# Optimization experiments

Measured on AMD Instinct MI355X. Metric: run time of the kernel, lower is better.

The kernel has to match this reference:

```python
import jax, jax.numpy as jnp
import numpy as np

B, S, W, D, T = 64, 512, 384, 768, 21


def setup_inputs() -> dict:
    key = jax.random.key(0)
    ks = jax.random.split(key, 8)
    hidden_states = jax.random.normal(ks[0], (B, S, D), dtype=jnp.float32)  # BERT last_hidden_state
    word_maps = jnp.sort(jax.random.randint(ks[1], (B, W), 0, S), axis=1)  # first-subword index per word
    tags = jax.random.randint(ks[2], (B, W), 0, T)
    word_mask = jnp.ones((B, W), dtype=bool)  # torchcrf requires mask[:,0] all on
    W_tag = jax.random.normal(ks[3], (T, D), dtype=jnp.float32) * 0.02  # hidden2tag weight
    b_tag = jnp.zeros((T,), dtype=jnp.float32)
    start_trans = jax.random.uniform(ks[4], (T,), minval=-0.1, maxval=0.1)
    end_trans = jax.random.uniform(ks[5], (T,), minval=-0.1, maxval=0.1)
    trans = jax.random.uniform(ks[6], (T, T), minval=-0.1, maxval=0.1)
    return dict(hidden_states=hidden_states, W_tag=W_tag, b_tag=b_tag,
                start_trans=start_trans, end_trans=end_trans, trans=trans,
                word_maps=word_maps, tags=tags, word_mask=word_mask)


def reference(hidden_states, W_tag, b_tag, start_trans, end_trans, trans,
              word_maps, tags, word_mask):
    # --- ragged subword -> word gather (vectorized form of the python loop) ---
    word_feats = jnp.take_along_axis(hidden_states, word_maps[:, :, None], axis=1)  # [B,W,D]
    # dropout is identity in eval / deterministic reference
    emissions = jnp.einsum('bwd,td->bwt', word_feats, W_tag) + b_tag  # [B,W,T]

    maskf = word_mask.astype(emissions.dtype)
    bidx = jnp.arange(tags.shape[0])

    # --- CRF numerator: score of the given tag sequence ---
    emit_sc = jnp.take_along_axis(emissions, tags[:, :, None], axis=2)[..., 0]  # [B,W]
    trans_sc = trans[tags[:, :-1], tags[:, 1:]]                                  # [B,W-1]
    num = start_trans[tags[:, 0]] + emit_sc[:, 0]
    num = num + jnp.sum((trans_sc + emit_sc[:, 1:]) * maskf[:, 1:], axis=1)
    lengths = word_mask.sum(axis=1)
    last_tags = jnp.take_along_axis(tags, (lengths - 1)[:, None], axis=1)[:, 0]
    num = num + end_trans[last_tags]

    # --- CRF denominator: log partition via forward recurrence (scan over time) ---
    def step(score, xm):
        em_t, m_t = xm  # [B,T], [B]
        nxt = jax.nn.logsumexp(score[:, :, None] + trans[None, :, :] + em_t[:, None, :], axis=1)
        return jnp.where(m_t[:, None], nxt, score), None

    score0 = start_trans[None, :] + emissions[:, 0]  # [B,T]
    score, _ = jax.lax.scan(step, score0,
                            (jnp.swapaxes(emissions[:, 1:], 0, 1), word_mask[:, 1:].T))
    log_z = jax.nn.logsumexp(score + end_trans[None, :], axis=1)  # [B]

    llh = num - log_z
    return -jnp.mean(llh)  # reduction='mean', negated
```

## Files before the change

### kernel.cpp

```cpp
#include <hip/hip_runtime.h>
#include <math.h>

#define BB 64
#define SS 512
#define WW 384
#define DD 768
#define TT 21
#define ROWS (BB*WW)
#define EMSTRIDE (WW*TT)
#define NCH 32
#define CLEN 12
#define PSTRIDE 24
#define LSTR 28
#define PTSZ (PSTRIDE*PSTRIDE)
#define LN32 3.4657359027997265f

typedef short   bf16x8 __attribute__((ext_vector_type(8)));
typedef float   f32x4  __attribute__((ext_vector_type(4)));
union FragU { bf16x8 v; unsigned u[4]; };

__device__ __forceinline__ unsigned pack_bf16(unsigned lo, unsigned hi) {
    return __builtin_amdgcn_perm(hi, lo, 0x07060302);
}

__global__ __launch_bounds__(256) void emissions_kernel(
    const float* __restrict__ hidden, const int* __restrict__ word_maps,
    const float* __restrict__ W_tag, const float* __restrict__ b_tag,
    float* __restrict__ em, float* __restrict__ out)
{
    __shared__ __align__(16) unsigned short Bs[24 * 2 * 4 * 16 * 8];
    __shared__ __align__(16) float Sred[2][64][8];
    __shared__ int rowoff[32];

    const int tid = threadIdx.x;
    const int rowBase = blockIdx.x * 32;

    if (blockIdx.x == 0 && tid == 0) out[0] = 0.0f;

    if (tid < 32) {
        int row = rowBase + tid;
        int b = row / WW;
        int w = row - b * WW;
        rowoff[tid] = b * SS + word_maps[b * WW + w];
    }

    for (int i = tid; i < TT * (DD / 4); i += 256) {
        int t = i / (DD / 4), q = i - t * (DD / 4);
        int k  = q * 4;
        int ks = k >> 5, quad = (k >> 3) & 3, e = k & 7;
        int nt = t >> 4, l16 = t & 15;
        float4 wv = *(const float4*)&W_tag[t * DD + k];
        int off = ((ks * 2 + nt) * 4 + quad) * 128 + l16 * 8 + e;
        *(unsigned*)&Bs[off]     = pack_bf16(__float_as_uint(wv.x), __float_as_uint(wv.y));
        *(unsigned*)&Bs[off + 2] = pack_bf16(__float_as_uint(wv.z), __float_as_uint(wv.w));
    }
    __syncthreads();

    const int wv_  = tid >> 6;
    const int rt   = wv_ >> 1;
    const int h    = wv_ & 1;
    const int lane = tid & 63;
    const int l16  = lane & 15;
    const int quad = lane >> 4;

    const float* abase = hidden + (size_t)rowoff[rt * 16 + l16] * DD
                                + h * (DD / 2) + quad * 8;
    const unsigned short* bbase = Bs + quad * 128 + l16 * 8 + h * 12 * 1024;

    f32x4 acc0 = {}, acc1 = {};

    float4 A0[4], A1[4];
    #pragma unroll
    for (int p = 0; p < 4; ++p) {
        A0[p] = *(const float4*)(abase + p * 32);
        A1[p] = *(const float4*)(abase + p * 32 + 4);
    }
    bf16x8 b0c = *(const bf16x8*)(bbase);
    bf16x8 b1c = *(const bf16x8*)(bbase + 512);

    #pragma unroll
    for (int ks = 0; ks < 12; ++ks) {
        bf16x8 b0n = b0c, b1n = b1c;
        if (ks < 11) {
            b0n = *(const bf16x8*)(bbase + (ks + 1) * 1024);
            b1n = *(const bf16x8*)(bbase + (ks + 1) * 1024 + 512);
        }
        FragU a;
        a.u[0] = pack_bf16(__float_as_uint(A0[ks & 3].x), __float_as_uint(A0[ks & 3].y));
        a.u[1] = pack_bf16(__float_as_uint(A0[ks & 3].z), __float_as_uint(A0[ks & 3].w));
        a.u[2] = pack_bf16(__float_as_uint(A1[ks & 3].x), __float_as_uint(A1[ks & 3].y));
        a.u[3] = pack_bf16(__float_as_uint(A1[ks & 3].z), __float_as_uint(A1[ks & 3].w));
        if (ks < 8) {
            A0[ks & 3] = *(const float4*)(abase + (ks + 4) * 32);
            A1[ks & 3] = *(const float4*)(abase + (ks + 4) * 32 + 4);
        }
        acc0 = __builtin_amdgcn_mfma_f32_16x16x32_bf16(a.v, b0c, acc0, 0, 0, 0);
        acc1 = __builtin_amdgcn_mfma_f32_16x16x32_bf16(a.v, b1c, acc1, 0, 0, 0);
        b0c = b0n; b1c = b1n;
    }

    if (h == 1) {
        #pragma unroll
        for (int r = 0; r < 4; ++r) {
            Sred[rt][lane][r]     = acc0[r];
            Sred[rt][lane][r + 4] = acc1[r];
        }
    }
    __syncthreads();

    if (h == 0) {
        #pragma unroll
        for (int r = 0; r < 4; ++r) {
            acc0[r] += Sred[rt][lane][r];
            acc1[r] += Sred[rt][lane][r + 4];
        }
        int rbase = rowBase + rt * 16 + quad * 4;
        {
            float bt = b_tag[l16];
            #pragma unroll
            for (int r = 0; r < 4; ++r)
                em[(size_t)(rbase + r) * TT + l16] = acc0[r] + bt;
        }
        if (16 + l16 < TT) {
            float bt = b_tag[16 + l16];
            #pragma unroll
            for (int r = 0; r < 4; ++r)
                em[(size_t)(rbase + r) * TT + 16 + l16] = acc1[r] + bt;
        }
    }
}

__global__ __launch_bounds__(256, 2) void chunk_kernel(
    const float* __restrict__ em, const float* __restrict__ trans,
    float* __restrict__ Pmat)
{
    __shared__ __align__(16) float Es[24 * LSTR];
    __shared__ __align__(16) float Pbuf[4][2][21 * LSTR];
    __shared__ __align__(16) float gem[4][CLEN * LSTR];

    const int tid  = threadIdx.x;
    const int wid  = tid >> 6;
    const int lane = tid & 63;
    const int id   = blockIdx.x * 4 + wid;
    const int b    = id / NCH;
    const int c    = id - b * NCH;
    const int s0   = 1 + c * CLEN;
    const int n    = (c == NCH - 1) ? (WW - s0) : CLEN;

    for (int idx = tid; idx < 24 * LSTR; idx += 256) {
        int k = idx / LSTR, j = idx - k * LSTR;
        Es[idx] = (k < TT && j < TT) ? __expf(trans[k * TT + j]) * 0.03125f : 0.f;
    }

    int i3r = lane / 6;
    const int jg  = lane - i3r * 6;
    const bool active = (i3r < 7) && (jg < 6);
    const int i3 = (i3r < 7) ? i3r : 6;
    const int jbase = (jg < 6 ? jg : 5) * 4;

    for (int idx = lane; idx < n * LSTR; idx += 64) {
        int tt = idx / LSTR, j = idx - tt * LSTR;
        float g = 1.0f;
        if (j < TT) g = __expf(em[((size_t)b * WW + (s0 + tt)) * TT + j]);
        gem[wid][idx] = g;
    }
    __syncthreads();

    float4 Er[24];
    #pragma unroll
    for (int k = 0; k < 24; ++k)
        Er[k] = *(const float4*)&Es[k * LSTR + jbase];

    {
        float4 g = *(const float4*)&gem[wid][jbase];
        #pragma unroll
        for (int r = 0; r < 3; ++r) {
            int i = i3 * 3 + r;
            float4 e = *(const float4*)&Es[i * LSTR + jbase];
            float4 v = make_float4(e.x * g.x, e.y * g.y, e.z * g.z, e.w * g.w);
            if (active) *(float4*)&Pbuf[wid][0][i * LSTR + jbase] = v;
        }
    }

    int pp = 0;
    for (int tt = 1; tt < n; ++tt) {
        float acc[3][4];
        #pragma unroll
        for (int r = 0; r < 3; ++r)
            #pragma unroll
            for (int q = 0; q < 4; ++q) acc[r][q] = 0.f;

        const float* Pc = &Pbuf[wid][pp][0];
        #pragma unroll
        for (int kb = 0; kb < 6; ++kb) {
            float4 p0 = *(const float4*)&Pc[(i3 * 3 + 0) * LSTR + kb * 4];
            float4 p1 = *(const float4*)&Pc[(i3 * 3 + 1) * LSTR + kb * 4];
            float4 p2 = *(const float4*)&Pc[(i3 * 3 + 2) * LSTR + kb * 4];
            #pragma unroll
            for (int kk = 0; kk < 4; ++kk) {
                float4 e = Er[kb * 4 + kk];
                float a = (kk == 0) ? p0.x : (kk == 1) ? p0.y : (kk == 2) ? p0.z : p0.w;
                float bv= (kk == 0) ? p1.x : (kk == 1) ? p1.y : (kk == 2) ? p1.z : p1.w;
                float cv= (kk == 0) ? p2.x : (kk == 1) ? p2.y : (kk == 2) ? p2.z : p2.w;
                acc[0][0] = fmaf(a, e.x, acc[0][0]); acc[0][1] = fmaf(a, e.y, acc[0][1]);
                acc[0][2] = fmaf(a, e.z, acc[0][2]); acc[0][3] = fmaf(a, e.w, acc[0][3]);
                acc[1][0] = fmaf(bv, e.x, acc[1][0]); acc[1][1] = fmaf(bv, e.y, acc[1][1]);
                acc[1][2] = fmaf(bv, e.z, acc[1][2]); acc[1][3] = fmaf(bv, e.w, acc[1][3]);
                acc[2][0] = fmaf(cv, e.x, acc[2][0]); acc[2][1] = fmaf(cv, e.y, acc[2][1]);
                acc[2][2] = fmaf(cv, e.z, acc[2][2]); acc[2][3] = fmaf(cv, e.w, acc[2][3]);
            }
        }
        float4 g = *(const float4*)&gem[wid][tt * LSTR + jbase];
        if (active) {
            #pragma unroll
            for (int r = 0; r < 3; ++r) {
                float4 v = make_float4(acc[r][0] * g.x, acc[r][1] * g.y,
                                       acc[r][2] * g.z, acc[r][3] * g.w);
                *(float4*)&Pbuf[wid][1 - pp][(i3 * 3 + r) * LSTR + jbase] = v;
            }
        }
        pp ^= 1;
    }

    float* dst = Pmat + (size_t)id * PTSZ;
    const float* Pf = &Pbuf[wid][pp][0];
    for (int idx = lane; idx < PTSZ; idx += 64) {
        int j = idx / PSTRIDE, i = idx - j * PSTRIDE;
        dst[idx] = (i < TT) ? Pf[i * LSTR + j] : 0.f;
    }
}

__device__ __forceinline__ float lane_bcast(float v, int l) {
    return __uint_as_float(__builtin_amdgcn_readlane(__float_as_uint(v), l));
}

#define LOADC(q0,q1,q2,q3,q4,q5,cc) { \
    const float* Pp = Pb + (size_t)(cc) * PTSZ; \
    q0 = *(const float4*)&Pp[0];  q1 = *(const float4*)&Pp[4]; \
    q2 = *(const float4*)&Pp[8];  q3 = *(const float4*)&Pp[12]; \
    q4 = *(const float4*)&Pp[16]; q5 = Pp[20]; }

#define MERGE(c_, q0,q1,q2,q3,q4,q5) { \
    float col[TT]; \
    col[0]=q0.x;  col[1]=q0.y;  col[2]=q0.z;  col[3]=q0.w; \
    col[4]=q1.x;  col[5]=q1.y;  col[6]=q1.z;  col[7]=q1.w; \
    col[8]=q2.x;  col[9]=q2.y;  col[10]=q2.z; col[11]=q2.w; \
    col[12]=q3.x; col[13]=q3.y; col[14]=q3.z; col[15]=q3.w; \
    col[16]=q4.x; col[17]=q4.y; col[18]=q4.z; col[19]=q4.w; \
    col[20]=q5; \
    float p0 = 0.f, p1 = 0.f, p2 = 0.f; \
    _Pragma("unroll") \
    for (int i = 0; i < TT; i += 3) { \
        p0 = fmaf(lane_bcast(sig, i    ), col[i    ], p0); \
        p1 = fmaf(lane_bcast(sig, i + 1), col[i + 1], p1); \
        p2 = fmaf(lane_bcast(sig, i + 2), col[i + 2], p2); \
    } \
    float v = act ? (p0 + p1 + p2) : 0.0f; \
    float m = v; \
    _Pragma("unroll") \
    for (int o = 32; o > 0; o >>= 1) m = fmaxf(m, __shfl_xor(m, o)); \
    int nst = ((c_) == NCH - 1) ? (WW - (1 + (c_) * CLEN)) : CLEN; \
    M += __logf(m) + (float)nst * LN32; \
    sig = v / m; }

__global__ __launch_bounds__(64, 1) void combine_kernel(
    const float* __restrict__ Pmat, const float* __restrict__ em,
    const int* __restrict__ tags, const float* __restrict__ start_trans,
    const float* __restrict__ end_trans, const float* __restrict__ trans,
    float* __restrict__ out)
{
    const int b = blockIdx.x;
    const int j = threadIdx.x;
    const bool act = (j < TT);
    const int jc = act ? j : (TT - 1);
    const float* emb = em + (size_t)b * EMSTRIDE;
    const float* Pb = Pmat + (size_t)b * NCH * PTSZ + jc * PSTRIDE;

    float4 A0,A1,A2,A3,A4; float A5;
    float4 B0,B1,B2,B3,B4; float B5;
    float4 C0,C1,C2,C3,C4; float C5;
    float4 D0,D1,D2,D3,D4; float D5;
    LOADC(A0,A1,A2,A3,A4,A5, 0);
    LOADC(B0,B1,B2,B3,B4,B5, 1);
    LOADC(C0,C1,C2,C3,C4,C5, 2);
    LOADC(D0,D1,D2,D3,D4,D5, 3);

    float s0v = start_trans[jc] + emb[jc];
    float M = act ? s0v : -1e30f;
    #pragma unroll
    for (int o = 32; o > 0; o >>= 1) M = fmaxf(M, __shfl_xor(M, o));
    float sig = act ? __expf(s0v - M) : 0.0f;

    for (int c = 0; c < NCH; c += 4) {
        MERGE(c,     A0,A1,A2,A3,A4,A5);
        if (c + 4 < NCH) LOADC(A0,A1,A2,A3,A4,A5, c + 4);
        MERGE(c + 1, B0,B1,B2,B3,B4,B5);
        if (c + 5 < NCH) LOADC(B0,B1,B2,B3,B4,B5, c + 5);
        MERGE(c + 2, C0,C1,C2,C3,C4,C5);
        if (c + 6 < NCH) LOADC(C0,C1,C2,C3,C4,C5, c + 6);
        MERGE(c + 3, D0,D1,D2,D3,D4,D5);
        if (c + 7 < NCH) LOADC(D0,D1,D2,D3,D4,D5, c + 7);
    }

    float fin = (act && sig > 0.f) ? (M + __logf(sig) + end_trans[jc]) : -1e30f;
    float mm = fin;
    #pragma unroll
    for (int o = 32; o > 0; o >>= 1) mm = fmaxf(mm, __shfl_xor(mm, o));
    float pe = __expf(fin - mm);
    float ssum = pe;
    #pragma unroll
    for (int o = 32; o > 0; o >>= 1) ssum += __shfl_xor(ssum, o);
    float lz = mm + __logf(ssum);

    const int* tb = tags + b * WW;
    float part = 0.f;
    #pragma unroll
    for (int w = j; w < WW; w += 64) {
        int tw = tb[w];
        float e = emb[w * TT + tw];
        float tsc = (w == 0) ? start_trans[tw] : trans[tb[w - 1] * TT + tw];
        part += tsc + e;
    }
    #pragma unroll
    for (int o = 32; o > 0; o >>= 1) part += __shfl_xor(part, o);

    if (j == 0) {
        float num = part + end_trans[tb[WW - 1]];
        atomicAdd(out, -(num - lz) * (1.0f / BB));
    }
}

extern "C" void kernel_launch(void* const* d_in, const int* in_sizes, int n_in,
                              void* d_out, int out_size, void* d_ws, size_t ws_size,
                              hipStream_t stream) {
    const float* hidden      = (const float*)d_in[0];
    const float* W_tag       = (const float*)d_in[1];
    const float* b_tag       = (const float*)d_in[2];
    const float* start_trans = (const float*)d_in[3];
    const float* end_trans   = (const float*)d_in[4];
    const float* trans       = (const float*)d_in[5];
    const int*   word_maps   = (const int*)  d_in[6];
    const int*   tags        = (const int*)  d_in[7];

    float* out  = (float*)d_out;
    float* em   = (float*)d_ws;
    float* Pmat = (float*)d_ws + (size_t)ROWS * TT;

    emissions_kernel<<<ROWS / 32, 256, 0, stream>>>(hidden, word_maps, W_tag, b_tag, em, out);
    chunk_kernel<<<BB * NCH / 4, 256, 0, stream>>>(em, trans, Pmat);
    combine_kernel<<<BB, 64, 0, stream>>>(Pmat, em, tags, start_trans, end_trans, trans, out);
}
```

Measured before the change: 196.9 us.

## Fuse combine kernel into chunk kernel via last-block-done counter per batch

Drops the separate combine kernel launch. Each chunk block bumps a per-batch atomic counter after writing its partial transfer matrices, and the last of the 8 blocks for that batch runs the merge and log-likelihood reduction. The emissions kernel zeroes the counters. This removes one kernel launch and its dependency gap. The cost is a threadfence, an extra barrier, and a serial merge tail running on a single wave.

Result: slower. 238.2 us (+21.0%).

```diff
diff --git a/kernel.cpp b/kernel.cpp
--- a/kernel.cpp
+++ b/kernel.cpp
@@ -26,7 +26,7 @@
 __global__ __launch_bounds__(256) void emissions_kernel(
     const float* __restrict__ hidden, const int* __restrict__ word_maps,
     const float* __restrict__ W_tag, const float* __restrict__ b_tag,
-    float* __restrict__ em, float* __restrict__ out)
+    float* __restrict__ em, float* __restrict__ out, int* __restrict__ cnt)
 {
     __shared__ __align__(16) unsigned short Bs[24 * 2 * 4 * 16 * 8];
     __shared__ __align__(16) float Sred[2][64][8];
@@ -35,7 +35,10 @@
     const int tid = threadIdx.x;
     const int rowBase = blockIdx.x * 32;
 
-    if (blockIdx.x == 0 && tid == 0) out[0] = 0.0f;
+    if (blockIdx.x == 0) {
+        if (tid == 0) out[0] = 0.0f;
+        if (tid < BB) cnt[tid] = 0;
+    }
 
     if (tid < 32) {
         int row = rowBase + tid;
@@ -127,106 +130,6 @@
             for (int r = 0; r < 4; ++r)
                 em[(size_t)(rbase + r) * TT + 16 + l16] = acc1[r] + bt;
         }
-    }
-}
-
-__global__ __launch_bounds__(256, 2) void chunk_kernel(
-    const float* __restrict__ em, const float* __restrict__ trans,
-    float* __restrict__ Pmat)
-{
-    __shared__ __align__(16) float Es[24 * LSTR];
-    __shared__ __align__(16) float Pbuf[4][2][21 * LSTR];
-    __shared__ __align__(16) float gem[4][CLEN * LSTR];
-
-    const int tid  = threadIdx.x;
-    const int wid  = tid >> 6;
-    const int lane = tid & 63;
-    const int id   = blockIdx.x * 4 + wid;
-    const int b    = id / NCH;
-    const int c    = id - b * NCH;
-    const int s0   = 1 + c * CLEN;
-    const int n    = (c == NCH - 1) ? (WW - s0) : CLEN;
-
-    for (int idx = tid; idx < 24 * LSTR; idx += 256) {
-        int k = idx / LSTR, j = idx - k * LSTR;
-        Es[idx] = (k < TT && j < TT) ? __expf(trans[k * TT + j]) * 0.03125f : 0.f;
-    }
-
-    int i3r = lane / 6;
-    const int jg  = lane - i3r * 6;
-    const bool active = (i3r < 7) && (jg < 6);
-    const int i3 = (i3r < 7) ? i3r : 6;
-    const int jbase = (jg < 6 ? jg : 5) * 4;
-
-    for (int idx = lane; idx < n * LSTR; idx += 64) {
-        int tt = idx / LSTR, j = idx - tt * LSTR;
-        float g = 1.0f;
-        if (j < TT) g = __expf(em[((size_t)b * WW + (s0 + tt)) * TT + j]);
-        gem[wid][idx] = g;
-    }
-    __syncthreads();
-
-    float4 Er[24];
-    #pragma unroll
-    for (int k = 0; k < 24; ++k)
-        Er[k] = *(const float4*)&Es[k * LSTR + jbase];
-
-    {
-        float4 g = *(const float4*)&gem[wid][jbase];
-        #pragma unroll
-        for (int r = 0; r < 3; ++r) {
-            int i = i3 * 3 + r;
-            float4 e = *(const float4*)&Es[i * LSTR + jbase];
-            float4 v = make_float4(e.x * g.x, e.y * g.y, e.z * g.z, e.w * g.w);
-            if (active) *(float4*)&Pbuf[wid][0][i * LSTR + jbase] = v;
-        }
-    }
-
-    int pp = 0;
-    for (int tt = 1; tt < n; ++tt) {
-        float acc[3][4];
-        #pragma unroll
-        for (int r = 0; r < 3; ++r)
-            #pragma unroll
-            for (int q = 0; q < 4; ++q) acc[r][q] = 0.f;
-
-        const float* Pc = &Pbuf[wid][pp][0];
-        #pragma unroll
-        for (int kb = 0; kb < 6; ++kb) {
-            float4 p0 = *(const float4*)&Pc[(i3 * 3 + 0) * LSTR + kb * 4];
-            float4 p1 = *(const float4*)&Pc[(i3 * 3 + 1) * LSTR + kb * 4];
-            float4 p2 = *(const float4*)&Pc[(i3 * 3 + 2) * LSTR + kb * 4];
-            #pragma unroll
-            for (int kk = 0; kk < 4; ++kk) {
-                float4 e = Er[kb * 4 + kk];
-                float a = (kk == 0) ? p0.x : (kk == 1) ? p0.y : (kk == 2) ? p0.z : p0.w;
-                float bv= (kk == 0) ? p1.x : (kk == 1) ? p1.y : (kk == 2) ? p1.z : p1.w;
-                float cv= (kk == 0) ? p2.x : (kk == 1) ? p2.y : (kk == 2) ? p2.z : p2.w;
-                acc[0][0] = fmaf(a, e.x, acc[0][0]); acc[0][1] = fmaf(a, e.y, acc[0][1]);
-                acc[0][2] = fmaf(a, e.z, acc[0][2]); acc[0][3] = fmaf(a, e.w, acc[0][3]);
-                acc[1][0] = fmaf(bv, e.x, acc[1][0]); acc[1][1] = fmaf(bv, e.y, acc[1][1]);
-                acc[1][2] = fmaf(bv, e.z, acc[1][2]); acc[1][3] = fmaf(bv, e.w, acc[1][3]);
-                acc[2][0] = fmaf(cv, e.x, acc[2][0]); acc[2][1] = fmaf(cv, e.y, acc[2][1]);
-                acc[2][2] = fmaf(cv, e.z, acc[2][2]); acc[2][3] = fmaf(cv, e.w, acc[2][3]);
-            }
-        }
-        float4 g = *(const float4*)&gem[wid][tt * LSTR + jbase];
-        if (active) {
-            #pragma unroll
-            for (int r = 0; r < 3; ++r) {
-                float4 v = make_float4(acc[r][0] * g.x, acc[r][1] * g.y,
-                                       acc[r][2] * g.z, acc[r][3] * g.w);
-                *(float4*)&Pbuf[wid][1 - pp][(i3 * 3 + r) * LSTR + jbase] = v;
-            }
-        }
-        pp ^= 1;
-    }
-
-    float* dst = Pmat + (size_t)id * PTSZ;
-    const float* Pf = &Pbuf[wid][pp][0];
-    for (int idx = lane; idx < PTSZ; idx += 64) {
-        int j = idx / PSTRIDE, i = idx - j * PSTRIDE;
-        dst[idx] = (i < TT) ? Pf[i * LSTR + j] : 0.f;
     }
 }
 
@@ -263,18 +166,127 @@
     M += __logf(m) + (float)nst * LN32; \
     sig = v / m; }
 
-__global__ __launch_bounds__(64, 1) void combine_kernel(
-    const float* __restrict__ Pmat, const float* __restrict__ em,
+__global__ __launch_bounds__(256, 2) void chunk_kernel(
+    const float* __restrict__ em, const float* __restrict__ trans,
+    float* __restrict__ Pmat,
     const int* __restrict__ tags, const float* __restrict__ start_trans,
-    const float* __restrict__ end_trans, const float* __restrict__ trans,
+    const float* __restrict__ end_trans, int* __restrict__ cnt,
     float* __restrict__ out)
 {
-    const int b = blockIdx.x;
-    const int j = threadIdx.x;
+    __shared__ __align__(16) float Es[24 * LSTR];
+    __shared__ __align__(16) float Pbuf[4][2][21 * LSTR];
+    __shared__ __align__(16) float gem[4][CLEN * LSTR];
+    __shared__ int lastFlag;
+
+    const int tid  = threadIdx.x;
+    const int wid  = tid >> 6;
+    const int lane = tid & 63;
+    const int id   = blockIdx.x * 4 + wid;
+    const int b    = id / NCH;
+    const int c    = id - b * NCH;
+    const int s0   = 1 + c * CLEN;
+    const int n    = (c == NCH - 1) ? (WW - s0) : CLEN;
+
+    for (int idx = tid; idx < 24 * LSTR; idx += 256) {
+        int k = idx / LSTR, j = idx - k * LSTR;
+        Es[idx] = (k < TT && j < TT) ? __expf(trans[k * TT + j]) * 0.03125f : 0.f;
+    }
+
+    int i3r = lane / 6;
+    const int jg  = lane - i3r * 6;
+    const bool active = (i3r < 7) && (jg < 6);
+    const int i3 = (i3r < 7) ? i3r : 6;
+    const int jbase = (jg < 6 ? jg : 5) * 4;
+
+    for (int idx = lane; idx < n * LSTR; idx += 64) {
+        int tt = idx / LSTR, j = idx - tt * LSTR;
+        float g = 1.0f;
+        if (j < TT) g = __expf(em[((size_t)b * WW + (s0 + tt)) * TT + j]);
+        gem[wid][idx] = g;
+    }
+    __syncthreads();
+
+    float4 Er[24];
+    #pragma unroll
+    for (int k = 0; k < 24; ++k)
+        Er[k] = *(const float4*)&Es[k * LSTR + jbase];
+
+    {
+        float4 g = *(const float4*)&gem[wid][jbase];
+        #pragma unroll
+        for (int r = 0; r < 3; ++r) {
+            int i = i3 * 3 + r;
+            float4 e = *(const float4*)&Es[i * LSTR + jbase];
+            float4 v = make_float4(e.x * g.x, e.y * g.y, e.z * g.z, e.w * g.w);
+            if (active) *(float4*)&Pbuf[wid][0][i * LSTR + jbase] = v;
+        }
+    }
+
+    int pp = 0;
+    for (int tt = 1; tt < n; ++tt) {
+        float acc[3][4];
+        #pragma unroll
+        for (int r = 0; r < 3; ++r)
+            #pragma unroll
+            for (int q = 0; q < 4; ++q) acc[r][q] = 0.f;
+
+        const float* Pc = &Pbuf[wid][pp][0];
+        #pragma unroll
+        for (int kb = 0; kb < 6; ++kb) {
+            float4 p0 = *(const float4*)&Pc[(i3 * 3 + 0) * LSTR + kb * 4];
+            float4 p1 = *(const float4*)&Pc[(i3 * 3 + 1) * LSTR + kb * 4];
+            float4 p2 = *(const float4*)&Pc[(i3 * 3 + 2) * LSTR + kb * 4];
+            #pragma unroll
+            for (int kk = 0; kk < 4; ++kk) {
+                float4 e = Er[kb * 4 + kk];
+                float a = (kk == 0) ? p0.x : (kk == 1) ? p0.y : (kk == 2) ? p0.z : p0.w;
+                float bv= (kk == 0) ? p1.x : (kk == 1) ? p1.y : (kk == 2) ? p1.z : p1.w;
+                float cv= (kk == 0) ? p2.x : (kk == 1) ? p2.y : (kk == 2) ? p2.z : p2.w;
+                acc[0][0] = fmaf(a, e.x, acc[0][0]); acc[0][1] = fmaf(a, e.y, acc[0][1]);
+                acc[0][2] = fmaf(a, e.z, acc[0][2]); acc[0][3] = fmaf(a, e.w, acc[0][3]);
+                acc[1][0] = fmaf(bv, e.x, acc[1][0]); acc[1][1] = fmaf(bv, e.y, acc[1][1]);
+                acc[1][2] = fmaf(bv, e.z, acc[1][2]); acc[1][3] = fmaf(bv, e.w, acc[1][3]);
+                acc[2][0] = fmaf(cv, e.x, acc[2][0]); acc[2][1] = fmaf(cv, e.y, acc[2][1]);
+                acc[2][2] = fmaf(cv, e.z, acc[2][2]); acc[2][3] = fmaf(cv, e.w, acc[2][3]);
+            }
+        }
+        float4 g = *(const float4*)&gem[wid][tt * LSTR + jbase];
+        if (active) {
+            #pragma unroll
+            for (int r = 0; r < 3; ++r) {
+                float4 v = make_float4(acc[r][0] * g.x, acc[r][1] * g.y,
+                                       acc[r][2] * g.z, acc[r][3] * g.w);
+                *(float4*)&Pbuf[wid][1 - pp][(i3 * 3 + r) * LSTR + jbase] = v;
+            }
+        }
+        pp ^= 1;
+    }
+
+    {
+        float* dst = Pmat + (size_t)id * PTSZ;
+        const float* Pf = &Pbuf[wid][pp][0];
+        for (int idx = lane; idx < PTSZ; idx += 64) {
+            int j = idx / PSTRIDE, i = idx - j * PSTRIDE;
+            dst[idx] = (i < TT) ? Pf[i * LSTR + j] : 0.f;
+        }
+    }
+
+    __threadfence();
+    __syncthreads();
+    if (tid == 0) {
+        int prev = atomicAdd(&cnt[blockIdx.x >> 3], 1);
+        lastFlag = (prev == 7);
+    }
+    __syncthreads();
+    if (!lastFlag || tid >= 64) return;
+    __threadfence();
+
+    const int bb = blockIdx.x >> 3;
+    const int j = tid;
     const bool act = (j < TT);
     const int jc = act ? j : (TT - 1);
-    const float* emb = em + (size_t)b * EMSTRIDE;
-    const float* Pb = Pmat + (size_t)b * NCH * PTSZ + jc * PSTRIDE;
+    const float* emb = em + (size_t)bb * EMSTRIDE;
+    const float* Pb = Pmat + (size_t)bb * NCH * PTSZ + jc * PSTRIDE;
 
     float4 A0,A1,A2,A3,A4; float A5;
     float4 B0,B1,B2,B3,B4; float B5;
@@ -291,15 +303,15 @@
     for (int o = 32; o > 0; o >>= 1) M = fmaxf(M, __shfl_xor(M, o));
     float sig = act ? __expf(s0v - M) : 0.0f;
 
-    for (int c = 0; c < NCH; c += 4) {
-        MERGE(c,     A0,A1,A2,A3,A4,A5);
-        if (c + 4 < NCH) LOADC(A0,A1,A2,A3,A4,A5, c + 4);
-        MERGE(c + 1, B0,B1,B2,B3,B4,B5);
-        if (c + 5 < NCH) LOADC(B0,B1,B2,B3,B4,B5, c + 5);
-        MERGE(c + 2, C0,C1,C2,C3,C4,C5);
-        if (c + 6 < NCH) LOADC(C0,C1,C2,C3,C4,C5, c + 6);
-        MERGE(c + 3, D0,D1,D2,D3,D4,D5);
-        if (c + 7 < NCH) LOADC(D0,D1,D2,D3,D4,D5, c + 7);
+    for (int cc = 0; cc < NCH; cc += 4) {
+        MERGE(cc,     A0,A1,A2,A3,A4,A5);
+        if (cc + 4 < NCH) LOADC(A0,A1,A2,A3,A4,A5, cc + 4);
+        MERGE(cc + 1, B0,B1,B2,B3,B4,B5);
+        if (cc + 5 < NCH) LOADC(B0,B1,B2,B3,B4,B5, cc + 5);
+        MERGE(cc + 2, C0,C1,C2,C3,C4,C5);
+        if (cc + 6 < NCH) LOADC(C0,C1,C2,C3,C4,C5, cc + 6);
+        MERGE(cc + 3, D0,D1,D2,D3,D4,D5);
+        if (cc + 7 < NCH) LOADC(D0,D1,D2,D3,D4,D5, cc + 7);
     }
 
     float fin = (act && sig > 0.f) ? (M + __logf(sig) + end_trans[jc]) : -1e30f;
@@ -312,7 +324,7 @@
     for (int o = 32; o > 0; o >>= 1) ssum += __shfl_xor(ssum, o);
     float lz = mm + __logf(ssum);
 
-    const int* tb = tags + b * WW;
+    const int* tb = tags + bb * WW;
     float part = 0.f;
     #pragma unroll
     for (int w = j; w < WW; w += 64) {
@@ -327,6 +339,7 @@
     if (j == 0) {
         float num = part + end_trans[tb[WW - 1]];
         atomicAdd(out, -(num - lz) * (1.0f / BB));
+        cnt[bb] = 0;
     }
 }
 
@@ -345,8 +358,11 @@
     float* out  = (float*)d_out;
     float* em   = (float*)d_ws;
     float* Pmat = (float*)d_ws + (size_t)ROWS * TT;
-
-    emissions_kernel<<<ROWS / 32, 256, 0, stream>>>(hidden, word_maps, W_tag, b_tag, em, out);
-    chunk_kernel<<<BB * NCH / 4, 256, 0, stream>>>(em, trans, Pmat);
-    combine_kernel<<<BB, 64, 0, stream>>>(Pmat, em, tags, start_trans, end_trans, trans, out);
-}
+    int*   cnt  = (int*)((float*)d_ws + (size_t)ROWS * TT
+                         + (size_t)BB * NCH * PTSZ);
+
+    emissions_kernel<<<ROWS / 32, 256, 0, stream>>>(hidden, word_maps, W_tag, b_tag,
+                                                    em, out, cnt);
+    chunk_kernel<<<BB * NCH / 4, 256, 0, stream>>>(em, trans, Pmat, tags, start_trans,
+                                                   end_trans, cnt, out);
+}
```
